# Performance work log

Hardware: AMD Instinct MI355X
Metric: run time of the kernel (lower is better)

## Reference

```python
import jax, jax.numpy as jnp
import numpy as np

N = 100000   # nodes
E = 1600000  # edges
F = 64       # node_features


def setup_inputs() -> dict:
    key = jax.random.key(0)
    ks = jax.random.split(key, 8)
    x = jax.random.normal(ks[0], (N, F), dtype=jnp.float32)
    edge_index = jax.random.randint(ks[1], (2, E), 0, N, dtype=jnp.int64)
    edge_weight = jax.random.uniform(ks[2], (E,), dtype=jnp.float32)
    # degrees consistent with the graph (in-degree + 1 to avoid zeros)
    deg = jax.ops.segment_sum(jnp.ones((E,), jnp.float32), edge_index[1], num_segments=N) + 1.0
    W_init = jax.random.normal(ks[3], (F, F), dtype=jnp.float32) / np.sqrt(F)
    gru_wih = jax.random.normal(ks[4], (3 * F, F), dtype=jnp.float32) / np.sqrt(F)
    gru_whh = jax.random.normal(ks[5], (3 * F, F), dtype=jnp.float32) / np.sqrt(F)
    gru_bih = jnp.zeros((3 * F,), jnp.float32)
    gru_bhh = jnp.zeros((3 * F,), jnp.float32)
    lin_w = jax.random.normal(ks[6], (1, F), dtype=jnp.float32) / np.sqrt(F)
    lin_b = jnp.zeros((1,), jnp.float32)
    return {
        "x": x, "edge_index": edge_index, "edge_weight": edge_weight,
        "deg": deg, "target_num": N, "W_init": W_init,
        "gru_wih": gru_wih, "gru_whh": gru_whh,
        "gru_bih": gru_bih, "gru_bhh": gru_bhh,
        "lin_w": lin_w, "lin_b": lin_b,
    }


def _evolve_weight(W, wih, whh, bih, bhh):
    # EvolveGCN-O: GRU with the [F,F] weight matrix as both input and hidden.
    # Rows of W are the "batch"; PyTorch GRU gate order: r, z, n.
    gx = W @ wih.T + bih   # [F, 3F]
    gh = W @ whh.T + bhh   # [F, 3F]
    gx_r, gx_z, gx_n = jnp.split(gx, 3, axis=-1)
    gh_r, gh_z, gh_n = jnp.split(gh, 3, axis=-1)
    r = jax.nn.sigmoid(gx_r + gh_r)
    z = jax.nn.sigmoid(gx_z + gh_z)
    n = jnp.tanh(gx_n + r * gh_n)
    return (1.0 - z) * n + z * W


def reference(x, edge_index, edge_weight, deg, target_num, W_init,
              gru_wih, gru_whh, gru_bih, gru_bhh, lin_w, lin_b):
    # 1) evolve GCN weight with GRU
    W = _evolve_weight(W_init, gru_wih, gru_whh, gru_bih, gru_bhh)
    # 2) GCN conv with fixed evolved W: sym-normalized gather-scatter
    src, dst = edge_index[0], edge_index[1]
    dinv = jax.lax.rsqrt(deg)                       # [N]
    norm = edge_weight * dinv[src] * dinv[dst]      # [E]
    xw = x @ W                                      # [N, F]
    msgs = norm[:, None] * xw[src]                  # [E, F] (irregular gather)
    h = jax.ops.segment_sum(msgs, dst, num_segments=x.shape[0])  # scatter-add
    # 3) keep target nodes, ReLU, linear projection to 1
    h = jax.nn.relu(h[:target_num])
    out = h @ lin_w.T + lin_b                       # [target_num, 1]
    return out
```

## Files before the change

kernel.cpp:

```cpp
#include <hip/hip_runtime.h>
#include <hip/hip_bf16.h>

#define F 64
#define RB 128
#define RBSH 7
#define NBMAX 800
#define CHUNKA 8192
#define CAPR  2816
#define CAPL  3200
#define RCC   6

typedef int            nt_int4   __attribute__((ext_vector_type(4)));
typedef float          nt_float4 __attribute__((ext_vector_type(4)));

__device__ __forceinline__ unsigned short f2bf(float f) {
    unsigned int u = __float_as_uint(f);
    unsigned int r = (u + 0x7FFFu + ((u >> 16) & 1u)) >> 16;
    return (unsigned short)r;
}
__device__ __forceinline__ unsigned int pack2bf(float lo, float hi) {
    return (unsigned int)f2bf(lo) | ((unsigned int)f2bf(hi) << 16);
}

__global__ void evolve_kernel(const float* __restrict__ W,
                              const float* __restrict__ wih,
                              const float* __restrict__ whh,
                              const float* __restrict__ bih,
                              const float* __restrict__ bhh,
                              float* __restrict__ wt,
                              int* __restrict__ gcur, int NB) {
    if (blockIdx.x < 4) {
        int gi = blockIdx.x * 256 + threadIdx.x;
        if (gi < NB) gcur[gi] = gi * CAPR;
    }
    int t = blockIdx.x * blockDim.x + threadIdx.x;
    if (t >= F * F) return;
    int i = t >> 6;
    int j = t & 63;
    const float* Wi = W + i * F;
    float gxr = bih[j], gxz = bih[F + j], gxn = bih[2 * F + j];
    float ghr = bhh[j], ghz = bhh[F + j], ghn = bhh[2 * F + j];
#pragma unroll
    for (int k = 0; k < F; ++k) {
        float wv = Wi[k];
        gxr += wv * wih[(j) * F + k];
        gxz += wv * wih[(F + j) * F + k];
        gxn += wv * wih[(2 * F + j) * F + k];
        ghr += wv * whh[(j) * F + k];
        ghz += wv * whh[(F + j) * F + k];
        ghn += wv * whh[(2 * F + j) * F + k];
    }
    float r = 1.0f / (1.0f + expf(-(gxr + ghr)));
    float z = 1.0f / (1.0f + expf(-(gxz + ghz)));
    float n = tanhf(gxn + r * ghn);
    float wnew = (1.0f - z) * n + z * Wi[j];
    wt[j * F + i] = wnew;
}

__global__ void __launch_bounds__(256, 1) xw_kernel(
        const float* __restrict__ x,
        const float* __restrict__ wt,
        const float* __restrict__ deg,
        unsigned short* __restrict__ xw16, int N) {
    int i = blockIdx.x;
    int rowblk  = (i >> 5) * 8 + (i & 7);
    int quarter = (i >> 3) & 3;
    int r = rowblk * 256 + threadIdx.x;
    if (r >= N) return;
    float xr[F];
    const nt_float4* xp = (const nt_float4*)(x + (size_t)r * F);
#pragma unroll
    for (int q = 0; q < F / 4; ++q) {
        nt_float4 v = xp[q];
        xr[4 * q + 0] = v.x; xr[4 * q + 1] = v.y;
        xr[4 * q + 2] = v.z; xr[4 * q + 3] = v.w;
    }
    float dinv = rsqrtf(deg[r]);
    const float* wbase = wt + quarter * 16 * F;
    unsigned int o[8];
#pragma unroll
    for (int cb = 0; cb < 4; ++cb) {
        const float* w0 = wbase + (4 * cb) * F;
        float a0 = 0.f, a1 = 0.f, a2 = 0.f, a3 = 0.f;
#pragma unroll
        for (int k = 0; k < F; ++k) {
            float xv = xr[k];
            a0 += xv * w0[k];
            a1 += xv * w0[F + k];
            a2 += xv * w0[2 * F + k];
            a3 += xv * w0[3 * F + k];
        }
        o[2 * cb]     = pack2bf(a0 * dinv, a1 * dinv);
        o[2 * cb + 1] = pack2bf(a2 * dinv, a3 * dinv);
    }
    nt_int4* dst = (nt_int4*)(xw16 + (size_t)r * F + quarter * 16);
#pragma unroll
    for (int q = 0; q < 2; ++q) {
        nt_int4 v;
        v.x = (int)o[4 * q + 0]; v.y = (int)o[4 * q + 1];
        v.z = (int)o[4 * q + 2]; v.w = (int)o[4 * q + 3];
        dst[q] = v;
    }
}

__global__ void __launch_bounds__(1024) passA_kernel(
        const int* __restrict__ ei, const float* __restrict__ ew,
        int* __restrict__ gcur,
        unsigned long long* __restrict__ rec, int E, int NB) {
    __shared__ int lh[NBMAX];
    __shared__ int lcur[NBMAX];
    int t = threadIdx.x;
    for (int i = t; i < NB; i += 1024) lh[i] = 0;
    __syncthreads();
    int base = blockIdx.x * CHUNKA;
#pragma unroll
    for (int it = 0; it < CHUNKA / 1024; ++it) {
        int e = base + it * 1024 + t;
        if (e < E) atomicAdd(&lh[ei[E + e] >> RBSH], 1);
    }
    __syncthreads();
    for (int i = t; i < NB; i += 1024) {
        int c = lh[i];
        lcur[i] = c ? atomicAdd(&gcur[i], c) : 0;
    }
    __syncthreads();
#pragma unroll
    for (int it = 0; it < CHUNKA / 1024; ++it) {
        int e = base + it * 1024 + t;
        if (e < E) {
            int dst = ei[E + e];
            int src = ei[e];
            float w = ew[e];
            unsigned int q = (unsigned int)(w * 32767.0f + 0.5f);
            int b = dst >> RBSH;
            int p = atomicAdd(&lcur[b], 1);
            unsigned long long r = ((unsigned long long)(dst & (RB - 1)) << 32)
                                 | ((unsigned long long)((unsigned int)src) << 15) | q;
            rec[p] = r;
        }
    }
}

__global__ void __launch_bounds__(512) sortsum_kernel(
        const unsigned long long* __restrict__ rec,
        const int* __restrict__ gcur,
        const unsigned short* __restrict__ xw16,
        const float* __restrict__ deg,
        const float* __restrict__ lw,
        const float* __restrict__ lb,
        float* __restrict__ out, int M) {
    __shared__ unsigned int s_rec[CAPL];
    __shared__ int cnt[RB];
    __shared__ int pex[RB];
    __shared__ int cur[RB];
    int b = blockIdx.x;
    int t = threadIdx.x;
    int beg = b * CAPR;
    int end = gcur[b];

    for (int i = t; i < CAPL; i += 512) s_rec[i] = 0u;
    if (t < RB) cnt[t] = 0;
    __syncthreads();

    unsigned long long rc[RCC];
#pragma unroll
    for (int k = 0; k < RCC; ++k) {
        int i = beg + k * 512 + t;
        bool v = (i < end);
        rc[k] = v ? rec[i] : 0ull;
        if (v) atomicAdd(&cnt[(int)(rc[k] >> 32)], 1);
    }
    __syncthreads();

    if (t < RB) pex[t] = (cnt[t] + 3) & ~3;
    __syncthreads();
    for (int o = 1; o < RB; o <<= 1) {
        int v = (t < RB && t >= o) ? pex[t - o] : 0;
        __syncthreads();
        if (t < RB) pex[t] += v;
        __syncthreads();
    }
    if (t < RB) {
        int pcnt = (cnt[t] + 3) & ~3;
        int excl = pex[t] - pcnt;
        pex[t] = excl;
        cur[t] = excl;
    }
    __syncthreads();

#pragma unroll
    for (int k = 0; k < RCC; ++k) {
        int i = beg + k * 512 + t;
        if (i < end) {
            int dl = (int)(rc[k] >> 32);
            int p = atomicAdd(&cur[dl], 1);
            s_rec[p] = (unsigned int)rc[k];
        }
    }
    __syncthreads();

    int lane = t & 63;
    int wv = t >> 6;
    int eg = lane >> 4;
    int fq = lane & 15;
    unsigned int flo = (unsigned int)(fq << 3);
    const char* xb = (const char*)xw16;
    float lw0 = lw[4 * fq + 0], lw1 = lw[4 * fq + 1];
    float lw2 = lw[4 * fq + 2], lw3 = lw[4 * fq + 3];
    const float esc = 1.0f / 32767.0f;
    int node0 = b << RBSH;
    for (int nl = wv; nl < RB; nl += 8) {
        int node = node0 + nl;
        if (node >= M) break;
        int nbeg = pex[nl];
        int iters = (cnt[nl] + 3) >> 2;
        float a0 = 0.f, a1 = 0.f, a2 = 0.f, a3 = 0.f;
#pragma unroll 4
        for (int i = 0; i < iters; ++i) {
            unsigned int r = s_rec[nbeg + 4 * i + eg];
            unsigned int off = ((r >> 8) & 0xFFFFFF80u) + flo;
            uint2 u = *(const uint2*)(xb + off);
            float q = (float)(r & 32767u);
            a0 += q * __uint_as_float(u.x << 16);
            a1 += q * __uint_as_float(u.x & 0xFFFF0000u);
            a2 += q * __uint_as_float(u.y << 16);
            a3 += q * __uint_as_float(u.y & 0xFFFF0000u);
        }
        a0 += __shfl_xor(a0, 16, 64); a0 += __shfl_xor(a0, 32, 64);
        a1 += __shfl_xor(a1, 16, 64); a1 += __shfl_xor(a1, 32, 64);
        a2 += __shfl_xor(a2, 16, 64); a2 += __shfl_xor(a2, 32, 64);
        a3 += __shfl_xor(a3, 16, 64); a3 += __shfl_xor(a3, 32, 64);
        float s = fmaxf(a0, 0.f) * lw0 + fmaxf(a1, 0.f) * lw1
                + fmaxf(a2, 0.f) * lw2 + fmaxf(a3, 0.f) * lw3;
#pragma unroll
        for (int o = 8; o; o >>= 1) s += __shfl_xor(s, o, 64);
        if (lane == 0) out[node] = s * (esc * rsqrtf(deg[node])) + lb[0];
    }
}

extern "C" void kernel_launch(void* const* d_in, const int* in_sizes, int n_in,
                              void* d_out, int out_size, void* d_ws, size_t ws_size,
                              hipStream_t stream) {
    const float* x   = (const float*)d_in[0];
    const int*   ei  = (const int*)d_in[1];
    const float* ew  = (const float*)d_in[2];
    const float* deg = (const float*)d_in[3];
    const float* W0  = (const float*)d_in[5];
    const float* wih = (const float*)d_in[6];
    const float* whh = (const float*)d_in[7];
    const float* bih = (const float*)d_in[8];
    const float* bhh = (const float*)d_in[9];
    const float* lw  = (const float*)d_in[10];
    const float* lb  = (const float*)d_in[11];
    float* out = (float*)d_out;

    int N = in_sizes[0] / F;
    int E = in_sizes[1] / 2;
    int M = out_size;
    int NB = (N + RB - 1) / RB;

    float*              wt   = (float*)d_ws;
    unsigned short*     xw16 = (unsigned short*)(wt + 8192);
    unsigned long long* rec  = (unsigned long long*)(xw16 + (size_t)N * F);
    int*                gcur = (int*)(rec + (size_t)NB * CAPR);

    evolve_kernel<<<(F * F + 255) / 256, 256, 0, stream>>>(W0, wih, whh, bih, bhh, wt, gcur, NB);

    {
        int nrb8 = (((N + 255) / 256) + 7) & ~7;
        xw_kernel<<<4 * nrb8, 256, 0, stream>>>(x, wt, deg, xw16, N);
    }

    passA_kernel<<<(E + CHUNKA - 1) / CHUNKA, 1024, 0, stream>>>(ei, ew, gcur, rec, E, NB);

    sortsum_kernel<<<NB, 512, 0, stream>>>(rec, gcur, xw16, deg, lw, lb, out, M);
}
```

Measured before the change: 117.5 us.

## Split each destination bucket across two half-bucket blocks in sortsum

The sort-and-sum kernel now launches two 256-thread blocks per 128-node bucket, each filtering the bucket's records to its own 64-node half before the local counting sort and gather-reduce. This doubles the number of blocks and cuts shared memory per block, aiming at better occupancy and GPU fill. In exchange each bucket's record list is read twice from global memory and register use per thread rises.

```diff
diff --git a/kernel.cpp b/kernel.cpp
--- a/kernel.cpp
+++ b/kernel.cpp
@@ -7,8 +7,9 @@
 #define NBMAX 800
 #define CHUNKA 8192
 #define CAPR  2816
-#define CAPL  3200
-#define RCC   6
+#define HB 64
+#define CAPL  1792
+#define RCC   11
 
 typedef int            nt_int4   __attribute__((ext_vector_type(4)));
 typedef float          nt_float4 __attribute__((ext_vector_type(4)));
@@ -141,7 +142,7 @@
     }
 }
 
-__global__ void __launch_bounds__(512) sortsum_kernel(
+__global__ void __launch_bounds__(256) sortsum_kernel(
         const unsigned long long* __restrict__ rec,
         const int* __restrict__ gcur,
         const unsigned short* __restrict__ xw16,
@@ -150,37 +151,44 @@
         const float* __restrict__ lb,
         float* __restrict__ out, int M) {
     __shared__ unsigned int s_rec[CAPL];
-    __shared__ int cnt[RB];
-    __shared__ int pex[RB];
-    __shared__ int cur[RB];
-    int b = blockIdx.x;
+    __shared__ int cnt[HB];
+    __shared__ int pex[HB];
+    __shared__ int cur[HB];
+    int blk = blockIdx.x;
+    int bb = blk >> 1;
+    int h  = blk & 1;
     int t = threadIdx.x;
-    int beg = b * CAPR;
-    int end = gcur[b];
-
-    for (int i = t; i < CAPL; i += 512) s_rec[i] = 0u;
-    if (t < RB) cnt[t] = 0;
+    int beg = bb * CAPR;
+    int end = gcur[bb];
+
+    for (int i = t; i < CAPL; i += 256) s_rec[i] = 0u;
+    if (t < HB) cnt[t] = 0;
     __syncthreads();
 
     unsigned long long rc[RCC];
 #pragma unroll
     for (int k = 0; k < RCC; ++k) {
-        int i = beg + k * 512 + t;
+        int i = beg + k * 256 + t;
         bool v = (i < end);
-        rc[k] = v ? rec[i] : 0ull;
-        if (v) atomicAdd(&cnt[(int)(rc[k] >> 32)], 1);
-    }
-    __syncthreads();
-
-    if (t < RB) pex[t] = (cnt[t] + 3) & ~3;
-    __syncthreads();
-    for (int o = 1; o < RB; o <<= 1) {
-        int v = (t < RB && t >= o) ? pex[t - o] : 0;
+        rc[k] = v ? rec[i] : 0xFFFFFFFFFFFFFFFFull;
+        if (v) {
+            int dl = (int)(rc[k] >> 32);
+            if ((dl >> 6) == h) atomicAdd(&cnt[dl & (HB - 1)], 1);
+        } else {
+            rc[k] = 0xFFFFFFFFFFFFFFFFull;
+        }
+    }
+    __syncthreads();
+
+    if (t < HB) pex[t] = (cnt[t] + 3) & ~3;
+    __syncthreads();
+    for (int o = 1; o < HB; o <<= 1) {
+        int v = (t < HB && t >= o) ? pex[t - o] : 0;
         __syncthreads();
-        if (t < RB) pex[t] += v;
+        if (t < HB) pex[t] += v;
         __syncthreads();
     }
-    if (t < RB) {
+    if (t < HB) {
         int pcnt = (cnt[t] + 3) & ~3;
         int excl = pex[t] - pcnt;
         pex[t] = excl;
@@ -190,11 +198,13 @@
 
 #pragma unroll
     for (int k = 0; k < RCC; ++k) {
-        int i = beg + k * 512 + t;
-        if (i < end) {
-            int dl = (int)(rc[k] >> 32);
-            int p = atomicAdd(&cur[dl], 1);
-            s_rec[p] = (unsigned int)rc[k];
+        unsigned long long r = rc[k];
+        if (r != 0xFFFFFFFFFFFFFFFFull) {
+            int dl = (int)(r >> 32);
+            if ((dl >> 6) == h) {
+                int p = atomicAdd(&cur[dl & (HB - 1)], 1);
+                s_rec[p] = (unsigned int)r;
+            }
         }
     }
     __syncthreads();
@@ -208,8 +218,8 @@
     float lw0 = lw[4 * fq + 0], lw1 = lw[4 * fq + 1];
     float lw2 = lw[4 * fq + 2], lw3 = lw[4 * fq + 3];
     const float esc = 1.0f / 32767.0f;
-    int node0 = b << RBSH;
-    for (int nl = wv; nl < RB; nl += 8) {
+    int node0 = (bb << RBSH) + (h << 6);
+    for (int nl = wv; nl < HB; nl += 4) {
         int node = node0 + nl;
         if (node >= M) break;
         int nbeg = pex[nl];
@@ -273,5 +283,5 @@
 
     passA_kernel<<<(E + CHUNKA - 1) / CHUNKA, 1024, 0, stream>>>(ei, ew, gcur, rec, E, NB);
 
-    sortsum_kernel<<<NB, 512, 0, stream>>>(rec, gcur, xw16, deg, lw, lb, out, M);
-}
+    sortsum_kernel<<<2 * NB, 256, 0, stream>>>(rec, gcur, xw16, deg, lw, lb, out, M);
+}
```

Result: no change. 118.2 us (+0.6%).
